# Optimization experiments

Measured on AMD Instinct MI355X. Metric: run time of the kernel, lower is better.

Reference implementation:

```python
import jax, jax.numpy as jnp
import numpy as np

D_MODEL = 1024
NUM_HEADS = 16
D_K = D_MODEL // NUM_HEADS


def setup_inputs() -> dict:
    key = jax.random.key(0)
    ks = jax.random.split(key, 9)
    s = 1.0 / np.sqrt(D_MODEL)
    x = jax.random.normal(ks[0], (1, 4096, D_MODEL), dtype=jnp.float32)
    Wq = jax.random.uniform(ks[1], (D_MODEL, D_MODEL), jnp.float32, -s, s)
    bq = jax.random.uniform(ks[2], (D_MODEL,), jnp.float32, -s, s)
    Wk = jax.random.uniform(ks[3], (D_MODEL, D_MODEL), jnp.float32, -s, s)
    bk = jax.random.uniform(ks[4], (D_MODEL,), jnp.float32, -s, s)
    Wv = jax.random.uniform(ks[5], (D_MODEL, D_MODEL), jnp.float32, -s, s)
    bv = jax.random.uniform(ks[6], (D_MODEL,), jnp.float32, -s, s)
    Wo = jax.random.uniform(ks[7], (D_MODEL, D_MODEL), jnp.float32, -s, s)
    bo = jax.random.uniform(ks[8], (D_MODEL,), jnp.float32, -s, s)
    return {"x": x, "Wq": Wq, "bq": bq, "Wk": Wk, "bk": bk,
            "Wv": Wv, "bv": bv, "Wo": Wo, "bo": bo}


def reference(x, Wq, bq, Wk, bk, Wv, bv, Wo, bo):
    B, S, _ = x.shape
    scale = jnp.sqrt(jnp.asarray(D_K, dtype=x.dtype))
    # projections (torch Linear: y = x @ W.T + b)
    q = (x @ Wq.T + bq).reshape(B, S, NUM_HEADS, D_K).transpose(0, 2, 1, 3)
    k = (x @ Wk.T + bk).reshape(B, S, NUM_HEADS, D_K).transpose(0, 2, 1, 3)
    v = (x @ Wv.T + bv).reshape(B, S, NUM_HEADS, D_K).transpose(0, 2, 1, 3)
    # [B, H, S, S] naive scores, causal mask, softmax
    scores = jnp.einsum('bhqd,bhkd->bhqk', q, k) / scale
    causal = jnp.tril(jnp.ones((S, S), dtype=bool))
    scores = jnp.where(causal, scores, jnp.asarray(-jnp.inf, dtype=scores.dtype))
    probs = jax.nn.softmax(scores, axis=-1)
    out = jnp.einsum('bhqk,bhkd->bhqd', probs, v)
    out = out.transpose(0, 2, 1, 3).reshape(B, S, D_MODEL)
    return out @ Wo.T + bo
```

## Files before the change

### kernel.cpp

```cpp
#include <hip/hip_runtime.h>
#include <math.h>

#define SEQ 4096
#define DMODEL 1024
#define NH 16
#define DK 64
#define LDP 72

typedef __bf16    bf16x8 __attribute__((ext_vector_type(8)));
typedef float     f32x4  __attribute__((ext_vector_type(4)));
typedef __fp16    fp16x2 __attribute__((ext_vector_type(2)));
typedef _Float16  h16x2  __attribute__((ext_vector_type(2)));
typedef _Float16  h16x4  __attribute__((ext_vector_type(4)));
typedef _Float16  h16x8  __attribute__((ext_vector_type(8)));

#define GLOAD_LDS16(g, l) __builtin_amdgcn_global_load_lds(                     \
    (const __attribute__((address_space(1))) unsigned int*)(g),                 \
    (__attribute__((address_space(3))) unsigned int*)(l), 16, 0, 0)

__device__ __forceinline__ h16x2 cvt_pk_h16(float a, float b) {
    fp16x2 r = __builtin_amdgcn_cvt_pkrtz(a, b);
    return __builtin_bit_cast(h16x2, r);
}

__global__ __launch_bounds__(256)
void cvt_all(const float* __restrict__ x, const float* __restrict__ Wq,
             const float* __restrict__ Wk, const float* __restrict__ Wv,
             const float* __restrict__ Wo, __bf16* __restrict__ dst)
{
    const size_t M1 = 1u << 20;
    const size_t e = ((size_t)blockIdx.x * 256 + threadIdx.x) * 8;
    const float* src; size_t off;
    if      (e < 4*M1) { src = x;  off = e;        }
    else if (e < 5*M1) { src = Wq; off = e - 4*M1; }
    else if (e < 6*M1) { src = Wk; off = e - 5*M1; }
    else if (e < 7*M1) { src = Wv; off = e - 6*M1; }
    else               { src = Wo; off = e - 7*M1; }
    const float4 f0 = *reinterpret_cast<const float4*>(&src[off]);
    const float4 f1 = *reinterpret_cast<const float4*>(&src[off + 4]);
    bf16x8 pk;
    pk[0]=(__bf16)f0.x; pk[1]=(__bf16)f0.y; pk[2]=(__bf16)f0.z; pk[3]=(__bf16)f0.w;
    pk[4]=(__bf16)f1.x; pk[5]=(__bf16)f1.y; pk[6]=(__bf16)f1.z; pk[7]=(__bf16)f1.w;
    *reinterpret_cast<bf16x8*>(&dst[e]) = pk;
}

__device__ __forceinline__ void gemm_core128(const __bf16* __restrict__ A,
                                             const __bf16* __restrict__ W,
                                             int m0, int n0, int t,
                                             __bf16* AsF, __bf16* BsF,
                                             f32x4 acc[4][4])
{
    const int w = t >> 6, lane = t & 63, l15 = lane & 15, quad = lane >> 4;
    const int wm = (w & 1) * 64, wn = (w >> 1) * 64;
    const int lr = lane >> 3, lc = lane & 7;
    for (int k0 = 0; k0 < DMODEL; k0 += 64) {
        __syncthreads();
        #pragma unroll
        for (int p = 0; p < 4; ++p) {
            const int n = w*4 + p;
            const int r = n*8 + lr;
            const int cl = lc ^ (r & 7);
            GLOAD_LDS16(&A[(size_t)(m0 + r) * DMODEL + k0 + cl*8], &AsF[n*512]);
            GLOAD_LDS16(&W[(size_t)(n0 + r) * DMODEL + k0 + cl*8], &BsF[n*512]);
        }
        __syncthreads();
        #pragma unroll
        for (int kb = 0; kb < 2; ++kb) {
            const int phys = ((kb*4 + quad) ^ (l15 & 7)) * 8;
            bf16x8 af[4], bfr[4];
            #pragma unroll
            for (int i = 0; i < 4; ++i) {
                af[i]  = *reinterpret_cast<const bf16x8*>(&AsF[(wm + i*16 + l15)*64 + phys]);
                bfr[i] = *reinterpret_cast<const bf16x8*>(&BsF[(wn + i*16 + l15)*64 + phys]);
            }
            #pragma unroll
            for (int ms = 0; ms < 4; ++ms)
                #pragma unroll
                for (int ns = 0; ns < 4; ++ns)
                    acc[ms][ns] = __builtin_amdgcn_mfma_f32_16x16x32_bf16(af[ms], bfr[ns], acc[ms][ns], 0, 0, 0);
        }
    }
}

__global__ __launch_bounds__(256, 3)
void gemm_qkv(const __bf16* __restrict__ xb, const __bf16* __restrict__ Wcat,
              const float* __restrict__ bq, const float* __restrict__ bk,
              const float* __restrict__ bv,
              _Float16* __restrict__ Qh, _Float16* __restrict__ Kh, _Float16* __restrict__ Vth)
{
    __shared__ __bf16 SM[4*64*LDP];
    __bf16* AsF = SM;
    __bf16* BsF = SM + 8192;
    const int t = threadIdx.x;
    const int n0g = blockIdx.x * 128;
    const int m0  = blockIdx.y * 128;
    const int which = n0g >> 10;
    const int n_in  = n0g & 1023;

    f32x4 acc[4][4] = {};
    gemm_core128(xb, Wcat, m0, n0g, t, AsF, BsF, acc);

    const int w = t >> 6, lane = t & 63, l15 = lane & 15, quad = lane >> 4;
    const int wm = (w & 1) * 64, wn = (w >> 1) * 64;
    const float* bias = (which == 0) ? bq : (which == 1) ? bk : bv;
    float br[4];
    #pragma unroll
    for (int ns = 0; ns < 4; ++ns) br[ns] = bias[n_in + wn + ns*16 + l15];

    if (which == 2) {
        #pragma unroll
        for (int ms = 0; ms < 4; ++ms)
            #pragma unroll
            for (int ns = 0; ns < 4; ++ns) {
                h16x4 pk;
                #pragma unroll
                for (int rg = 0; rg < 4; ++rg) pk[rg] = (_Float16)(acc[ms][ns][rg] + br[ns]);
                *reinterpret_cast<h16x4*>(
                    &Vth[(size_t)(n_in + wn + ns*16 + l15) * SEQ + m0 + wm + ms*16 + quad*4]) = pk;
            }
    } else {
        const float s = (which == 0) ? 0.1803368787f : 1.0f;
        _Float16* C = (which == 0) ? Qh : Kh;
        __syncthreads();
        _Float16* tile = (_Float16*)SM + w * 64 * LDP;
        #pragma unroll
        for (int ms = 0; ms < 4; ++ms)
            #pragma unroll
            for (int ns = 0; ns < 4; ++ns)
                #pragma unroll
                for (int rg = 0; rg < 4; ++rg)
                    tile[(ms*16 + quad*4 + rg) * LDP + ns*16 + l15] =
                        (_Float16)((acc[ms][ns][rg] + br[ns]) * s);
        asm volatile("s_waitcnt lgkmcnt(0)" ::: "memory");
        const int er = lane >> 3, ec = (lane & 7) * 8;
        #pragma unroll
        for (int p = 0; p < 8; ++p) {
            const h16x8 v = *reinterpret_cast<const h16x8*>(&tile[(er + p*8) * LDP + ec]);
            *reinterpret_cast<h16x8*>(
                &C[(size_t)(m0 + wm + er + p*8) * DMODEL + n_in + wn + ec]) = v;
        }
    }
}

__device__ __forceinline__ void gemm_core64(const __bf16* __restrict__ A,
                                            const __bf16* __restrict__ W,
                                            int m0, int n0, int t,
                                            __bf16* AsF, __bf16* BsF,
                                            f32x4 acc[2][4])
{
    const int w = t >> 6, lane = t & 63, l15 = lane & 15, quad = lane >> 4;
    const int lr = lane >> 3, lc = lane & 7;
    for (int k0 = 0; k0 < DMODEL; k0 += 64) {
        __syncthreads();
        #pragma unroll
        for (int p = 0; p < 4; ++p) {
            const int n = w*4 + p;
            const int r = n*8 + lr;
            const int cl = lc ^ (r & 7);
            GLOAD_LDS16(&A[(size_t)(m0 + r) * DMODEL + k0 + cl*8], &AsF[n*512]);
        }
        #pragma unroll
        for (int p = 0; p < 2; ++p) {
            const int n = w*2 + p;
            const int r = n*8 + lr;
            const int cl = lc ^ (r & 7);
            GLOAD_LDS16(&W[(size_t)(n0 + r) * DMODEL + k0 + cl*8], &BsF[n*512]);
        }
        __syncthreads();
        #pragma unroll
        for (int kb = 0; kb < 2; ++kb) {
            const int phys = ((kb*4 + quad) ^ (l15 & 7)) * 8;
            bf16x8 af0 = *reinterpret_cast<const bf16x8*>(&AsF[(w*32 + l15)*64 + phys]);
            bf16x8 af1 = *reinterpret_cast<const bf16x8*>(&AsF[(w*32 + 16 + l15)*64 + phys]);
            #pragma unroll
            for (int ns = 0; ns < 4; ++ns) {
                const bf16x8 bfr = *reinterpret_cast<const bf16x8*>(&BsF[(ns*16 + l15)*64 + phys]);
                acc[0][ns] = __builtin_amdgcn_mfma_f32_16x16x32_bf16(af0, bfr, acc[0][ns], 0, 0, 0);
                acc[1][ns] = __builtin_amdgcn_mfma_f32_16x16x32_bf16(af1, bfr, acc[1][ns], 0, 0, 0);
            }
        }
    }
}

__global__ __launch_bounds__(256, 4)
void gemm_out(const __bf16* __restrict__ Ob, const __bf16* __restrict__ Wob,
              const float* __restrict__ bo, float* __restrict__ out)
{
    __shared__ __bf16 AsF[128*64];
    __shared__ __bf16 BsF[64*64];
    const int t = threadIdx.x;
    const int n0 = blockIdx.x * 64;
    const int m0 = blockIdx.y * 128;

    f32x4 acc[2][4] = {};
    gemm_core64(Ob, Wob, m0, n0, t, AsF, BsF, acc);

    const int lane = t & 63, l15 = lane & 15, quad = lane >> 4, w = t >> 6;
    float br[4];
    #pragma unroll
    for (int ns = 0; ns < 4; ++ns) br[ns] = bo[n0 + ns*16 + l15];
    #pragma unroll
    for (int ms = 0; ms < 2; ++ms)
        #pragma unroll
        for (int ns = 0; ns < 4; ++ns)
            #pragma unroll
            for (int rg = 0; rg < 4; ++rg)
                out[(size_t)(m0 + w*32 + ms*16 + quad*4 + rg) * DMODEL + n0 + ns*16 + l15] =
                    acc[ms][ns][rg] + br[ns];
}

__global__ __launch_bounds__(256, 3)
void attn_mfma(const _Float16* __restrict__ Q, const _Float16* __restrict__ K,
               const _Float16* __restrict__ Vt, __bf16* __restrict__ O,
               float* __restrict__ part, float* __restrict__ lpart)
{
    __shared__ _Float16 KsF[2][64*64];
    __shared__ _Float16 VsF[2][64*64];

    const int t = threadIdx.x;
    const int w = t >> 6;
    const int lane = t & 63, l15 = lane & 15, quad = lane >> 4;
    const int lr = lane >> 3, lc = lane & 7;
    const int h = blockIdx.y;
    const int u = blockIdx.x;
    int qt, g;
    if      (u < 16) { qt = 16 + u; g = 0; }
    else if (u < 32) { qt = u;      g = 1; }
    else             { qt = 47 - u; g = 0; }
    const int tstart = g * 32;
    const int tlast  = 2*qt + 1;
    const int tend   = (tlast < tstart + 31) ? tlast : (tstart + 31);
    const int s0 = qt*128 + w*16;
    const int s1 = s0 + 64;

    h16x8 bq8[2][2];
    #pragma unroll
    for (int kb = 0; kb < 2; ++kb) {
        bq8[0][kb] = *reinterpret_cast<const h16x8*>(
            &Q[(size_t)(s0 + l15) * DMODEL + h*DK + kb*32 + quad*8]);
        bq8[1][kb] = *reinterpret_cast<const h16x8*>(
            &Q[(size_t)(s1 + l15) * DMODEL + h*DK + kb*32 + quad*8]);
    }

    const int cl = lc ^ lr;
    const int rA = (w*2 + 0)*8 + lr, rB = (w*2 + 1)*8 + lr;
    const int dA = (w*2 + 0)*512,   dB = (w*2 + 1)*512;
    const _Float16* kpA = &K [(size_t)(tstart*64 + rA) * DMODEL + h*DK + cl*8];
    const _Float16* kpB = &K [(size_t)(tstart*64 + rB) * DMODEL + h*DK + cl*8];
    const _Float16* vpA = &Vt[(size_t)(h*DK + rA) * SEQ + tstart*64 + cl*8];
    const _Float16* vpB = &Vt[(size_t)(h*DK + rB) * SEQ + tstart*64 + cl*8];

#define STAGE_KV(bi) do {                                     \
        GLOAD_LDS16(kpA, &KsF[bi][dA]);                       \
        GLOAD_LDS16(kpB, &KsF[bi][dB]);                       \
        GLOAD_LDS16(vpA, &VsF[bi][dA]);                       \
        GLOAD_LDS16(vpB, &VsF[bi][dB]);                       \
        kpA += (size_t)64*DMODEL; kpB += (size_t)64*DMODEL;   \
        vpA += 64; vpB += 64; } while (0)

    f32x4 acc[2][4] = {};
    f32x4 accl[2] = {};
    const h16x4 vone = {(_Float16)1.f, (_Float16)1.f, (_Float16)1.f, (_Float16)1.f};

    STAGE_KV(0);
    __syncthreads();

    int pbuf = 0;
    for (int tk = tstart; tk <= tend; ++tk, pbuf ^= 1) {
        if (tk < tend) STAGE_KV(pbuf ^ 1);

        const int j0 = tk * 64;
        const bool act0 = (j0 <= s0 + 15);
        const bool msk0 = (j0 + 63 > s0);
        const bool msk1 = (j0 + 63 > s1);
        const int rel0 = s0 - j0 + l15;
        const int rel1 = s1 - j0 + l15;

        h16x4 ap[2][4];
        #pragma unroll
        for (int st = 0; st < 4; ++st) {
            const h16x8 ak0 = *reinterpret_cast<const h16x8*>(
                &KsF[pbuf][(st*16 + l15)*64 + ((quad ^ (l15 & 7)))*8]);
            const h16x8 ak1 = *reinterpret_cast<const h16x8*>(
                &KsF[pbuf][(st*16 + l15)*64 + (((4 + quad) ^ (l15 & 7)))*8]);
            {
                f32x4 cc = {0.f, 0.f, 0.f, 0.f};
                cc = __builtin_amdgcn_mfma_f32_16x16x32_f16(ak0, bq8[1][0], cc, 0, 0, 0);
                cc = __builtin_amdgcn_mfma_f32_16x16x32_f16(ak1, bq8[1][1], cc, 0, 0, 0);
                float pv[4];
                #pragma unroll
                for (int rg = 0; rg < 4; ++rg) {
                    float e = exp2f(cc[rg]);
                    if (msk1 && (st*16 + quad*4 + rg > rel1)) e = 0.f;
                    pv[rg] = e;
                }
                const h16x2 lo = cvt_pk_h16(pv[0], pv[1]);
                const h16x2 hi = cvt_pk_h16(pv[2], pv[3]);
                ap[1][st] = (h16x4){lo[0], lo[1], hi[0], hi[1]};
                accl[1] = __builtin_amdgcn_mfma_f32_16x16x16f16(ap[1][st], vone, accl[1], 0, 0, 0);
            }
            if (act0) {
                f32x4 cc = {0.f, 0.f, 0.f, 0.f};
                cc = __builtin_amdgcn_mfma_f32_16x16x32_f16(ak0, bq8[0][0], cc, 0, 0, 0);
                cc = __builtin_amdgcn_mfma_f32_16x16x32_f16(ak1, bq8[0][1], cc, 0, 0, 0);
                float pv[4];
                #pragma unroll
                for (int rg = 0; rg < 4; ++rg) {
                    float e = exp2f(cc[rg]);
                    if (msk0 && (st*16 + quad*4 + rg > rel0)) e = 0.f;
                    pv[rg] = e;
                }
                const h16x2 lo = cvt_pk_h16(pv[0], pv[1]);
                const h16x2 hi = cvt_pk_h16(pv[2], pv[3]);
                ap[0][st] = (h16x4){lo[0], lo[1], hi[0], hi[1]};
                accl[0] = __builtin_amdgcn_mfma_f32_16x16x16f16(ap[0][st], vone, accl[0], 0, 0, 0);
            }
        }

        #pragma unroll
        for (int ds_ = 0; ds_ < 4; ++ds_) {
            #pragma unroll
            for (int st = 0; st < 4; ++st) {
                const h16x4 bv = *reinterpret_cast<const h16x4*>(
                    &VsF[pbuf][(ds_*16 + l15)*64 +
                               (((st*2 + (quad >> 1)) ^ (l15 & 7)))*8 + (quad & 1)*4]);
                acc[1][ds_] = __builtin_amdgcn_mfma_f32_16x16x16f16(ap[1][st], bv, acc[1][ds_], 0, 0, 0);
                if (act0)
                    acc[0][ds_] = __builtin_amdgcn_mfma_f32_16x16x16f16(ap[0][st], bv, acc[0][ds_], 0, 0, 0);
            }
        }
        __syncthreads();
    }
#undef STAGE_KV

    if (qt < 16) {
        #pragma unroll
        for (int s = 0; s < 2; ++s) {
            const int base = s ? s1 : s0;
            #pragma unroll
            for (int rg = 0; rg < 4; ++rg) {
                const float inv = 1.0f / accl[s][rg];
                const size_t row = (size_t)(base + quad*4 + rg) * DMODEL + h * DK;
                #pragma unroll
                for (int ds_ = 0; ds_ < 4; ++ds_)
                    O[row + ds_*16 + l15] = (__bf16)(acc[s][ds_][rg] * inv);
            }
        }
    } else {
        const int unit = (h*16 + (qt - 16))*2 + g;
        const size_t pbase = (size_t)unit * 8192;
        #pragma unroll
        for (int s = 0; s < 2; ++s) {
            #pragma unroll
            for (int rg = 0; rg < 4; ++rg) {
                const int lrow = s*64 + w*16 + quad*4 + rg;
                #pragma unroll
                for (int ds_ = 0; ds_ < 4; ++ds_)
                    part[pbase + lrow*64 + ds_*16 + l15] = acc[s][ds_][rg];
            }
            if (l15 == 0) {
                #pragma unroll
                for (int rg = 0; rg < 4; ++rg)
                    lpart[unit*128 + s*64 + w*16 + quad*4 + rg] = accl[s][rg];
            }
        }
    }
}

__global__ __launch_bounds__(256)
void attn_combine(const float* __restrict__ part, const float* __restrict__ lpart,
                  __bf16* __restrict__ O)
{
    const int t = threadIdx.x;
    const int qtp = blockIdx.x;
    const int h = blockIdx.y;
    const int u0 = (h*16 + qtp)*2;
    const size_t b0 = (size_t)u0 * 8192;
    const size_t b1 = b0 + 8192;
    const int r  = t >> 1;
    const int d0 = (t & 1) * 32;

    const float l = lpart[u0*128 + r] + lpart[(u0 + 1)*128 + r];
    const float inv = 1.0f / l;
    const size_t grow = (size_t)((16 + qtp)*128 + r) * DMODEL + h*64 + d0;
    #pragma unroll
    for (int i = 0; i < 4; ++i) {
        bf16x8 pk;
        #pragma unroll
        for (int j = 0; j < 2; ++j) {
            const float4 p0 = *reinterpret_cast<const float4*>(&part[b0 + r*64 + d0 + i*8 + j*4]);
            const float4 p1 = *reinterpret_cast<const float4*>(&part[b1 + r*64 + d0 + i*8 + j*4]);
            pk[j*4+0] = (__bf16)((p0.x + p1.x) * inv);
            pk[j*4+1] = (__bf16)((p0.y + p1.y) * inv);
            pk[j*4+2] = (__bf16)((p0.z + p1.z) * inv);
            pk[j*4+3] = (__bf16)((p0.w + p1.w) * inv);
        }
        *reinterpret_cast<bf16x8*>(&O[grow + i*8]) = pk;
    }
}

extern "C" void kernel_launch(void* const* d_in, const int* in_sizes, int n_in,
                              void* d_out, int out_size, void* d_ws, size_t ws_size,
                              hipStream_t stream) {
    const float* x  = (const float*)d_in[0];
    const float* Wq = (const float*)d_in[1];
    const float* bq = (const float*)d_in[2];
    const float* Wk = (const float*)d_in[3];
    const float* bk = (const float*)d_in[4];
    const float* Wv = (const float*)d_in[5];
    const float* bv = (const float*)d_in[6];
    const float* Wo = (const float*)d_in[7];
    const float* bo = (const float*)d_in[8];
    float* out = (float*)d_out;

    const size_t M1 = 1u << 20;
    __bf16* base = (__bf16*)d_ws;
    __bf16*    xb   = base;
    __bf16*    Wcat = base + 4*M1;
    __bf16*    Wob  = base + 7*M1;
    _Float16*  Qh   = (_Float16*)(base + 8*M1);
    _Float16*  Kh   = (_Float16*)(base + 12*M1);
    _Float16*  Vth  = (_Float16*)(base + 16*M1);
    __bf16*    Ob   = base + 20*M1;
    float*     lpart = (float*)(base + 24*M1);
    float*     part  = out;

    cvt_all<<<4096, 256, 0, stream>>>(x, Wq, Wk, Wv, Wo, base);
    gemm_qkv<<<dim3(24, 32), 256, 0, stream>>>(xb, Wcat, bq, bk, bv, Qh, Kh, Vth);
    attn_mfma<<<dim3(48, NH), 256, 0, stream>>>(Qh, Kh, Vth, Ob, part, lpart);
    attn_combine<<<dim3(16, NH), 256, 0, stream>>>(part, lpart, Ob);
    gemm_out<<<dim3(16, 32), 256, 0, stream>>>(Ob, Wob, bo, out);
}
```

Before: 229.2 us.

## Load K/V tiles directly from global into registers, dropping LDS staging

The attention kernel no longer stages K and V tiles into double-buffered shared memory with async global-to-LDS loads and barriers. Each wave now reads its own K and V fragments straight from global memory into registers every iteration. This removes the LDS traffic and the per-tile __syncthreads, but every wave (4 per block) fetches the same K/V data redundantly from L2/global. Load latency is also no longer hidden by prefetching the next tile.

```diff
diff --git a/kernel.cpp b/kernel.cpp
--- a/kernel.cpp
+++ b/kernel.cpp
@@ -214,13 +214,9 @@
                const _Float16* __restrict__ Vt, __bf16* __restrict__ O,
                float* __restrict__ part, float* __restrict__ lpart)
 {
-    __shared__ _Float16 KsF[2][64*64];
-    __shared__ _Float16 VsF[2][64*64];
-
     const int t = threadIdx.x;
     const int w = t >> 6;
     const int lane = t & 63, l15 = lane & 15, quad = lane >> 4;
-    const int lr = lane >> 3, lc = lane & 7;
     const int h = blockIdx.y;
     const int u = blockIdx.x;
     int qt, g;
@@ -242,33 +238,20 @@
             &Q[(size_t)(s1 + l15) * DMODEL + h*DK + kb*32 + quad*8]);
     }
 
-    const int cl = lc ^ lr;
-    const int rA = (w*2 + 0)*8 + lr, rB = (w*2 + 1)*8 + lr;
-    const int dA = (w*2 + 0)*512,   dB = (w*2 + 1)*512;
-    const _Float16* kpA = &K [(size_t)(tstart*64 + rA) * DMODEL + h*DK + cl*8];
-    const _Float16* kpB = &K [(size_t)(tstart*64 + rB) * DMODEL + h*DK + cl*8];
-    const _Float16* vpA = &Vt[(size_t)(h*DK + rA) * SEQ + tstart*64 + cl*8];
-    const _Float16* vpB = &Vt[(size_t)(h*DK + rB) * SEQ + tstart*64 + cl*8];
-
-#define STAGE_KV(bi) do {                                     \
-        GLOAD_LDS16(kpA, &KsF[bi][dA]);                       \
-        GLOAD_LDS16(kpB, &KsF[bi][dB]);                       \
-        GLOAD_LDS16(vpA, &VsF[bi][dA]);                       \
-        GLOAD_LDS16(vpB, &VsF[bi][dB]);                       \
-        kpA += (size_t)64*DMODEL; kpB += (size_t)64*DMODEL;   \
-        vpA += 64; vpB += 64; } while (0)
+    const _Float16* kp[4];
+    const _Float16* vp[4];
+    #pragma unroll
+    for (int st = 0; st < 4; ++st)
+        kp[st] = &K[(size_t)(tstart*64 + st*16 + l15) * DMODEL + h*DK + quad*8];
+    #pragma unroll
+    for (int ds_ = 0; ds_ < 4; ++ds_)
+        vp[ds_] = &Vt[(size_t)(h*DK + ds_*16 + l15) * SEQ + tstart*64 + quad*4];
 
     f32x4 acc[2][4] = {};
     f32x4 accl[2] = {};
     const h16x4 vone = {(_Float16)1.f, (_Float16)1.f, (_Float16)1.f, (_Float16)1.f};
 
-    STAGE_KV(0);
-    __syncthreads();
-
-    int pbuf = 0;
-    for (int tk = tstart; tk <= tend; ++tk, pbuf ^= 1) {
-        if (tk < tend) STAGE_KV(pbuf ^ 1);
-
+    for (int tk = tstart; tk <= tend; ++tk) {
         const int j0 = tk * 64;
         const bool act0 = (j0 <= s0 + 15);
         const bool msk0 = (j0 + 63 > s0);
@@ -276,17 +259,29 @@
         const int rel0 = s0 - j0 + l15;
         const int rel1 = s1 - j0 + l15;
 
+        h16x8 ak0v[4], ak1v[4];
+        h16x4 bvv[4][4];
+        #pragma unroll
+        for (int st = 0; st < 4; ++st) {
+            ak0v[st] = *reinterpret_cast<const h16x8*>(kp[st]);
+            ak1v[st] = *reinterpret_cast<const h16x8*>(kp[st] + 32);
+            kp[st] += (size_t)64 * DMODEL;
+        }
+        #pragma unroll
+        for (int ds_ = 0; ds_ < 4; ++ds_) {
+            #pragma unroll
+            for (int st = 0; st < 4; ++st)
+                bvv[ds_][st] = *reinterpret_cast<const h16x4*>(vp[ds_] + st*16);
+            vp[ds_] += 64;
+        }
+
         h16x4 ap[2][4];
         #pragma unroll
         for (int st = 0; st < 4; ++st) {
-            const h16x8 ak0 = *reinterpret_cast<const h16x8*>(
-                &KsF[pbuf][(st*16 + l15)*64 + ((quad ^ (l15 & 7)))*8]);
-            const h16x8 ak1 = *reinterpret_cast<const h16x8*>(
-                &KsF[pbuf][(st*16 + l15)*64 + (((4 + quad) ^ (l15 & 7)))*8]);
             {
                 f32x4 cc = {0.f, 0.f, 0.f, 0.f};
-                cc = __builtin_amdgcn_mfma_f32_16x16x32_f16(ak0, bq8[1][0], cc, 0, 0, 0);
-                cc = __builtin_amdgcn_mfma_f32_16x16x32_f16(ak1, bq8[1][1], cc, 0, 0, 0);
+                cc = __builtin_amdgcn_mfma_f32_16x16x32_f16(ak0v[st], bq8[1][0], cc, 0, 0, 0);
+                cc = __builtin_amdgcn_mfma_f32_16x16x32_f16(ak1v[st], bq8[1][1], cc, 0, 0, 0);
                 float pv[4];
                 #pragma unroll
                 for (int rg = 0; rg < 4; ++rg) {
@@ -301,8 +296,8 @@
             }
             if (act0) {
                 f32x4 cc = {0.f, 0.f, 0.f, 0.f};
-                cc = __builtin_amdgcn_mfma_f32_16x16x32_f16(ak0, bq8[0][0], cc, 0, 0, 0);
-                cc = __builtin_amdgcn_mfma_f32_16x16x32_f16(ak1, bq8[0][1], cc, 0, 0, 0);
+                cc = __builtin_amdgcn_mfma_f32_16x16x32_f16(ak0v[st], bq8[0][0], cc, 0, 0, 0);
+                cc = __builtin_amdgcn_mfma_f32_16x16x32_f16(ak1v[st], bq8[0][1], cc, 0, 0, 0);
                 float pv[4];
                 #pragma unroll
                 for (int rg = 0; rg < 4; ++rg) {
@@ -321,17 +316,12 @@
         for (int ds_ = 0; ds_ < 4; ++ds_) {
             #pragma unroll
             for (int st = 0; st < 4; ++st) {
-                const h16x4 bv = *reinterpret_cast<const h16x4*>(
-                    &VsF[pbuf][(ds_*16 + l15)*64 +
-                               (((st*2 + (quad >> 1)) ^ (l15 & 7)))*8 + (quad & 1)*4]);
-                acc[1][ds_] = __builtin_amdgcn_mfma_f32_16x16x16f16(ap[1][st], bv, acc[1][ds_], 0, 0, 0);
+                acc[1][ds_] = __builtin_amdgcn_mfma_f32_16x16x16f16(ap[1][st], bvv[ds_][st], acc[1][ds_], 0, 0, 0);
                 if (act0)
-                    acc[0][ds_] = __builtin_amdgcn_mfma_f32_16x16x16f16(ap[0][st], bv, acc[0][ds_], 0, 0, 0);
-            }
-        }
-        __syncthreads();
-    }
-#undef STAGE_KV
+                    acc[0][ds_] = __builtin_amdgcn_mfma_f32_16x16x16f16(ap[0][st], bvv[ds_][st], acc[0][ds_], 0, 0, 0);
+            }
+        }
+    }
 
     if (qt < 16) {
         #pragma unroll
```

Measured after the change: 329.6 us. 1.44x slower.
